# Kernel tuning notes

Measured on AMD Instinct MI355X. Metric: run time of the kernel, lower is better.

The kernel has to match this reference:

```python
import jax, jax.numpy as jnp
import numpy as np
import math

EPS = 1e-8
H, DM, S = 16, 1024, 128  # heads, d_model, seq_len (== channels)
DK = DM // H


def _fq_act_uint8(x):
    # Brevitas Uint8ActPerTensorFloat: per-tensor unsigned 8-bit fake-quant (negatives clip to 0)
    s = jnp.maximum(jnp.max(x), EPS) / 255.0
    return jnp.clip(jnp.round(x / s), 0.0, 255.0) * s


def _fq_w_int8(w):
    # Int8 weight per-tensor, narrow range [-127, 127]
    s = jnp.maximum(jnp.max(jnp.abs(w)), EPS) / 127.0
    return jnp.clip(jnp.round(w / s), -127.0, 127.0) * s, s


def _fq_pc_int8(x, axis):
    # QuantIdentity: signed 8-bit fake-quant, per-channel scale along `axis` (abs-max stats)
    red = tuple(i for i in range(x.ndim) if i != axis)
    s = jnp.maximum(jnp.max(jnp.abs(x), axis=red, keepdims=True), EPS) / 127.0
    return jnp.clip(jnp.round(x / s), -128.0, 127.0) * s


def _quant_linear(x, W, b):
    # QuantLinear: uint8 input quant, int8 weight quant, Int32 bias quant (scale = s_in * s_w)
    s_in = jnp.maximum(jnp.max(x), EPS) / 255.0
    xq = jnp.clip(jnp.round(x / s_in), 0.0, 255.0) * s_in
    Wq, s_w = _fq_w_int8(W)
    s_b = s_in * s_w
    bq = jnp.round(b / s_b) * s_b
    return jnp.einsum('bsd,od->bso', xq, Wq) + bq


def setup_inputs() -> dict:
    key = jax.random.key(0)
    ks = jax.random.split(key, 12)
    B = 64
    std = 1.0 / math.sqrt(DM)
    inp = {
        'query': jax.random.normal(ks[0], (B, S, DM), jnp.float32),
        'key':   jax.random.normal(ks[1], (B, S, DM), jnp.float32),
        'value': jax.random.normal(ks[2], (B, S, DM), jnp.float32),
        'mask':  jnp.ones((B, S, S), jnp.int32),
    }
    for i, nm in enumerate(['q', 'k', 'v', 'o']):
        inp[f'W{nm}'] = jax.random.normal(ks[3 + i], (DM, DM), jnp.float32) * std
        inp[f'b{nm}'] = jax.random.normal(ks[7 + i], (DM,), jnp.float32) * 0.01
    return inp


def reference(query, key, value, mask, Wq, bq, Wk, bk, Wv, bv, Wo, bo):
    B = query.shape[0]
    # QuantLinear projections -> [B, h, S, d_k]
    def proj(x, W, b):
        return _quant_linear(x, W, b).reshape(B, S, H, DK).transpose(0, 2, 1, 3)
    q = proj(query, Wq, bq)
    k = proj(key, Wk, bk)
    v = proj(value, Wv, bv)

    # quantizer_1: per-channel on q rows (axis 2); quantizer_2: on k^T columns (axis 3)
    kt = jnp.swapaxes(k, -2, -1)  # [B, h, d_k, S]
    scores = jnp.matmul(_fq_pc_int8(q, 2), _fq_pc_int8(kt, 3)) / math.sqrt(DK)
    scores = jnp.where(mask[:, None, :, :] == 0, -1e9, scores)
    p_attn = jax.nn.softmax(scores, axis=-1)

    # quantizer_3: per-channel on p_attn columns (axis 3); quantizer_4: on v rows (axis 2)
    x = jnp.matmul(_fq_pc_int8(p_attn, 3), _fq_pc_int8(v, 2))  # [B, h, S, d_k]
    x = x.transpose(0, 2, 1, 3).reshape(B, S, DM)
    return _quant_linear(x, Wo, bo)
```

## Files before the change

### kernel.cpp

```cpp
#include <hip/hip_runtime.h>
#include <hip/hip_bf16.h>
#include <math.h>

typedef unsigned short u16;
typedef unsigned int u32;
typedef unsigned long long u64;
typedef signed char i8;

constexpr int NB = 64, NS = 128, NDM = 1024, NH = 16, NDK = 64;
constexpr int NM = NB * NS;
constexpr float QEPS = 1e-8f;

typedef __attribute__((ext_vector_type(8))) short short8;
typedef __attribute__((ext_vector_type(4))) float f32x4;
typedef __attribute__((ext_vector_type(4))) int i32x4;

__device__ __forceinline__ u32 fenc(float f) {
  u32 u = __float_as_uint(f);
  return (u & 0x80000000u) ? ~u : (u | 0x80000000u);
}
__device__ __forceinline__ float fdec(u32 u) {
  u = (u & 0x80000000u) ? (u & 0x7FFFFFFFu) : ~u;
  return __uint_as_float(u);
}
__device__ __forceinline__ u16 f2bf(float f) { return (u16)(__float_as_uint(f) >> 16); }
__device__ __forceinline__ float bf2f(u16 u) { return __uint_as_float(((u32)u) << 16); }

__device__ __forceinline__ void glds16(const void* g, void* l) {
  __builtin_amdgcn_global_load_lds(
      (const __attribute__((address_space(1))) void*)(unsigned long long)(uintptr_t)g,
      (__attribute__((address_space(3))) void*)(u32)(uintptr_t)l, 16, 0, 0);
}


__global__ void init_kernel(u32* scl) {
  for (int i = threadIdx.x; i < 2048; i += blockDim.x) scl[i] = 0u;
}

__global__ void maskbits_kernel(const int* __restrict__ mask, u64* __restrict__ mb) {
  int row = blockIdx.x * 4 + (threadIdx.x >> 6);
  int lane = threadIdx.x & 63;
  const int* mrow = mask + (size_t)row * NS;
  u64 b0 = __ballot(mrow[lane] != 0);
  u64 b1 = __ballot(mrow[64 + lane] != 0);
  if (lane == 0) { mb[row * 2] = b0; mb[row * 2 + 1] = b1; }
}

__global__ void fused_max_kernel(const float* __restrict__ q, const float* __restrict__ k,
                                 const float* __restrict__ v, const float* __restrict__ w0,
                                 const float* __restrict__ w1, const float* __restrict__ w2,
                                 const float* __restrict__ w3, u32* __restrict__ sclu) {
  int y = blockIdx.y;
  const float* src; size_t n4; int ab;
  switch (y) {
    case 0: src = q; n4 = (size_t)NM * NDM / 4; ab = 0; break;
    case 1: src = k; n4 = (size_t)NM * NDM / 4; ab = 0; break;
    case 2: src = v; n4 = (size_t)NM * NDM / 4; ab = 0; break;
    case 3: src = w0; n4 = (size_t)NDM * NDM / 4; ab = 1; break;
    case 4: src = w1; n4 = (size_t)NDM * NDM / 4; ab = 1; break;
    case 5: src = w2; n4 = (size_t)NDM * NDM / 4; ab = 1; break;
    default: src = w3; n4 = (size_t)NDM * NDM / 4; ab = 1; break;
  }
  float m = -INFINITY;
  size_t stride = (size_t)gridDim.x * blockDim.x;
  for (size_t i = (size_t)blockIdx.x * blockDim.x + threadIdx.x; i < n4; i += stride) {
    float4 f = ((const float4*)src)[i];
    if (ab) { f.x = fabsf(f.x); f.y = fabsf(f.y); f.z = fabsf(f.z); f.w = fabsf(f.w); }
    m = fmaxf(m, fmaxf(fmaxf(f.x, f.y), fmaxf(f.z, f.w)));
  }
  for (int off = 32; off; off >>= 1) m = fmaxf(m, __shfl_down(m, off));
  __shared__ float sm[4];
  if ((threadIdx.x & 63) == 0) sm[threadIdx.x >> 6] = m;
  __syncthreads();
  if (threadIdx.x == 0) {
    float r = fmaxf(fmaxf(sm[0], sm[1]), fmaxf(sm[2], sm[3]));
    atomicMax(&sclu[y], fenc(r));
  }
}

__global__ __launch_bounds__(256)
void quant_w_i8_kernel(const float* __restrict__ w0, const float* __restrict__ w1,
                       const float* __restrict__ w2, const float* __restrict__ w3,
                       i8* __restrict__ dst, int* __restrict__ colsum,
                       const u32* __restrict__ sclu) {
  int y = blockIdx.y, row = blockIdx.x, tid = threadIdx.x;
  const float* src = (y == 0 ? w0 : y == 1 ? w1 : y == 2 ? w2 : w3) + (size_t)row * NDM;
  float s = fmaxf(fdec(sclu[3 + y]), QEPS) / 127.0f;
  float4 f = ((const float4*)src)[tid];
  int a = (int)fminf(fmaxf(rintf(f.x / s), -127.f), 127.f);
  int b = (int)fminf(fmaxf(rintf(f.y / s), -127.f), 127.f);
  int c = (int)fminf(fmaxf(rintf(f.z / s), -127.f), 127.f);
  int d = (int)fminf(fmaxf(rintf(f.w / s), -127.f), 127.f);
  ((int*)(dst + (size_t)y * NDM * NDM + (size_t)row * NDM))[tid] =
      (a & 255) | ((b & 255) << 8) | ((c & 255) << 16) | ((d & 255) << 24);
  int ssum = a + b + c + d;
  for (int off = 32; off; off >>= 1) ssum += __shfl_down(ssum, off);
  __shared__ int sm[4];
  if ((tid & 63) == 0) sm[tid >> 6] = ssum;
  __syncthreads();
  if (tid == 0) colsum[y * NDM + row] = sm[0] + sm[1] + sm[2] + sm[3];
}

__global__ void quant_a_kernel(const float* __restrict__ s0, const float* __restrict__ s1,
                               const float* __restrict__ s2, i8* __restrict__ dst,
                               const u32* __restrict__ sclu, int slot_base) {
  int y = blockIdx.y;
  const float* src = y == 0 ? s0 : y == 1 ? s1 : s2;
  i8* d = dst + (size_t)y * NM * NDM;
  float s = fmaxf(fdec(sclu[slot_base + y]), QEPS) / 255.0f;
  size_t n4 = (size_t)NM * NDM / 4;
  size_t stride = (size_t)gridDim.x * blockDim.x;
  for (size_t i = (size_t)blockIdx.x * blockDim.x + threadIdx.x; i < n4; i += stride) {
    float4 f = ((const float4*)src)[i];
    int a = (int)fminf(fmaxf(rintf(f.x / s), 0.f), 255.f) - 128;
    int b = (int)fminf(fmaxf(rintf(f.y / s), 0.f), 255.f) - 128;
    int c = (int)fminf(fmaxf(rintf(f.z / s), 0.f), 255.f) - 128;
    int e = (int)fminf(fmaxf(rintf(f.w / s), 0.f), 255.f) - 128;
    ((int*)d)[i] = (a & 255) | ((b & 255) << 8) | ((c & 255) << 16) | ((e & 255) << 24);
  }
}

__global__ void qkv_i8_kernel(const float* __restrict__ projbase, i8* __restrict__ dstbase,
                              const float* __restrict__ scl) {
  int y = blockIdx.y;
  const float* src = projbase + (size_t)y * NM * NDM;
  i8* dst = dstbase + (size_t)y * NM * NDM;
  const float* sb = scl + 8 + y * 128;
  size_t n4 = (size_t)NM * NDM / 4;
  size_t stride = (size_t)gridDim.x * blockDim.x;
  for (size_t i = (size_t)blockIdx.x * blockDim.x + threadIdx.x; i < n4; i += stride) {
    int s_idx = (int)((i >> 8) & 127);
    float s = fmaxf(sb[s_idx], QEPS) / 127.0f;
    float4 f = ((const float4*)src)[i];
    int a = (int)fminf(fmaxf(rintf(f.x / s), -128.f), 127.f);
    int b = (int)fminf(fmaxf(rintf(f.y / s), -128.f), 127.f);
    int c = (int)fminf(fmaxf(rintf(f.z / s), -128.f), 127.f);
    int d = (int)fminf(fmaxf(rintf(f.w / s), -128.f), 127.f);
    ((int*)dst)[i] = (a & 255) | ((b & 255) << 8) | ((c & 255) << 16) | ((d & 255) << 24);
  }
}

constexpr int BM = 128, BN = 128, BK = 64;

template <bool PROJ>
__global__ __launch_bounds__(256)
void gemm_kernel(const i8* __restrict__ Abase, const i8* __restrict__ Wbase,
                 const int* __restrict__ colsum, const float* __restrict__ b0,
                 const float* __restrict__ b1, const float* __restrict__ b2,
                 float* __restrict__ Cbase, u32* __restrict__ sclu) {
  constexpr int K = NDM, N = NDM;
  const int z = PROJ ? blockIdx.z : 0;
  const i8* A = Abase + (size_t)z * NM * NDM;
  const i8* Wt = PROJ ? (Wbase + (size_t)z * NDM * NDM) : Wbase;
  const float* bias = PROJ ? (z == 0 ? b0 : z == 1 ? b1 : b2) : b0;
  float* C = PROJ ? (Cbase + (size_t)z * NM * NDM) : Cbase;
  const u32* slot_in = PROJ ? (sclu + z) : (sclu + 7);
  const u32* slot_w = PROJ ? (sclu + 3 + z) : (sclu + 6);
  const int* cs = colsum + (PROJ ? z : 3) * NDM;

  __shared__ __align__(16) i8 As[BM][BK];
  __shared__ __align__(16) i8 Bs[BN][BK];
  __shared__ float rmax2[2][BM];

  const int tid = threadIdx.x;
  const int lane = tid & 63, wave = tid >> 6;
  const int wm = (wave & 1) * 64, wn = (wave >> 1) * 64;
  const int r16 = lane & 15, quad = lane >> 4;
  const int bm = blockIdx.x * BM, bn = blockIdx.y * BN;

  i32x4 acc[4][4] = {};

  const int lrow = lane >> 2, lcol = (lane & 3) * 16;
  for (int k0 = 0; k0 < K; k0 += BK) {
    __syncthreads();
#pragma unroll
    for (int p = 0; p < 2; p++) {
      int r = wave * 32 + p * 16;
      glds16(A + (size_t)(bm + r + lrow) * K + k0 + lcol, &As[r][0]);
      glds16(Wt + (size_t)(bn + r + lrow) * K + k0 + lcol, &Bs[r][0]);
    }
    __syncthreads();
    i32x4 af[4], bfr[4];
#pragma unroll
    for (int i = 0; i < 4; i++) af[i] = *(const i32x4*)(&As[wm + i * 16 + r16][quad * 16]);
#pragma unroll
    for (int j = 0; j < 4; j++) bfr[j] = *(const i32x4*)(&Bs[wn + j * 16 + r16][quad * 16]);
#pragma unroll
    for (int i = 0; i < 4; i++)
#pragma unroll
      for (int j = 0; j < 4; j++)
        acc[i][j] = __builtin_amdgcn_mfma_i32_16x16x64_i8(af[i], bfr[j], acc[i][j], 0, 0, 0);
  }

  float s_in = fmaxf(fdec(*slot_in), QEPS) / 255.0f;
  float s_w = fmaxf(fdec(*slot_w), QEPS) / 127.0f;
  float sc = s_in * s_w;

  float bq[4];
  int csj[4];
#pragma unroll
  for (int j = 0; j < 4; j++) {
    int gc = bn + wn + j * 16 + r16;
    bq[j] = rintf(bias[gc] / sc) * sc;
    csj[j] = cs[gc] << 7;
  }
#pragma unroll
  for (int i = 0; i < 4; i++) {
#pragma unroll
    for (int r = 0; r < 4; r++) {
      int lr = wm + i * 16 + quad * 4 + r;
      int gr = bm + lr;
      float rm = 0.0f;
#pragma unroll
      for (int j = 0; j < 4; j++) {
        int gc = bn + wn + j * 16 + r16;
        float val = (float)(acc[i][j][r] + csj[j]) * sc + bq[j];
        C[(size_t)gr * N + gc] = val;
        if (PROJ) rm = fmaxf(rm, fabsf(val));
      }
      if (PROJ) {
#pragma unroll
        for (int off = 1; off < 16; off <<= 1) rm = fmaxf(rm, __shfl_xor(rm, off));
        if (r16 == 0) rmax2[wave >> 1][lr] = rm;
      }
    }
  }
  if (PROJ) {
    __syncthreads();
    if (tid < BM) {
      float m = fmaxf(rmax2[0][tid], rmax2[1][tid]);
      atomicMax((int*)&sclu[8 + z * 128 + tid], __float_as_int(m));
    }
  }
}

__global__ __launch_bounds__(256)
void attn_scores_kernel(const i8* __restrict__ qi8, const i8* __restrict__ ki8,
                        const u64* __restrict__ mb, const float* __restrict__ scl,
                        u32* __restrict__ sclu, float* __restrict__ Pn) {
  const int bh = blockIdx.x, b = bh >> 4, h = bh & 15;
  const int tid = threadIdx.x, lane = tid & 63, wave = tid >> 6;
  const int r16 = lane & 15, quad = lane >> 4;

  __shared__ __align__(16) i8 Qs[NS][80];
  __shared__ __align__(16) i8 Ks[NS][80];
  __shared__ float sqv[NS], skv[NS];
  __shared__ float cmw[4][NS];

  {
    int row = tid >> 1, half = (tid & 1) * 32;
    const i8* qp = qi8 + (size_t)(b * NS + row) * NDM + h * NDK + half;
    const i8* kp = ki8 + (size_t)(b * NS + row) * NDM + h * NDK + half;
    *(int4*)&Qs[row][half] = *(const int4*)qp;
    *(int4*)&Qs[row][half + 16] = *(const int4*)(qp + 16);
    *(int4*)&Ks[row][half] = *(const int4*)kp;
    *(int4*)&Ks[row][half + 16] = *(const int4*)(kp + 16);
    if (tid < NS) {
      sqv[tid] = fmaxf(scl[8 + tid], QEPS) / 127.0f;
      skv[tid] = fmaxf(scl[8 + 128 + tid], QEPS) / 127.0f;
    }
  }
  __syncthreads();

  const int rowbase = wave * 32;
  i32x4 acc[2][8] = {};
#pragma unroll
  for (int mt = 0; mt < 2; mt++) {
    i32x4 a = *(const i32x4*)&Qs[rowbase + mt * 16 + r16][quad * 16];
#pragma unroll
    for (int nt = 0; nt < 8; nt++) {
      i32x4 bfrag = *(const i32x4*)&Ks[nt * 16 + r16][quad * 16];
      acc[mt][nt] = __builtin_amdgcn_mfma_i32_16x16x64_i8(a, bfrag, acc[mt][nt], 0, 0, 0);
    }
  }

  float skc[8], cm[8];
#pragma unroll
  for (int nt = 0; nt < 8; nt++) { skc[nt] = skv[nt * 16 + r16]; cm[nt] = 0.0f; }

#pragma unroll
  for (int mt = 0; mt < 2; mt++) {
#pragma unroll
    for (int r = 0; r < 4; r++) {
      int row = rowbase + mt * 16 + quad * 4 + r;
      float sq = sqv[row];
      const u64* mrow = mb + ((size_t)b * NS + row) * 2;
      u64 m0 = mrow[0], m1 = mrow[1];
      float vals[8];
      float mx = -INFINITY;
#pragma unroll
      for (int nt = 0; nt < 8; nt++) {
        float v = (float)acc[mt][nt][r] * (sq * skc[nt]) * 0.125f;
        u64 bits = nt < 4 ? m0 : m1;
        if (((bits >> ((nt * 16 + r16) & 63)) & 1ull) == 0) v = -1e9f;
        vals[nt] = v;
        mx = fmaxf(mx, v);
      }
#pragma unroll
      for (int off = 1; off < 16; off <<= 1) mx = fmaxf(mx, __shfl_xor(mx, off));
      float sum = 0.0f;
#pragma unroll
      for (int nt = 0; nt < 8; nt++) { vals[nt] = __expf(vals[nt] - mx); sum += vals[nt]; }
#pragma unroll
      for (int off = 1; off < 16; off <<= 1) sum += __shfl_xor(sum, off);
      float* prow = Pn + ((size_t)bh * NS + row) * NS;
#pragma unroll
      for (int nt = 0; nt < 8; nt++) {
        float p = vals[nt] / sum;
        prow[nt * 16 + r16] = p;
        cm[nt] = fmaxf(cm[nt], p);
      }
    }
  }

#pragma unroll
  for (int nt = 0; nt < 8; nt++) {
    float c = cm[nt];
    c = fmaxf(c, __shfl_xor(c, 16));
    c = fmaxf(c, __shfl_xor(c, 32));
    if (quad == 0) cmw[wave][nt * 16 + r16] = c;
  }
  __syncthreads();
  if (tid < NS) {
    float c = fmaxf(fmaxf(cmw[0][tid], cmw[1][tid]), fmaxf(cmw[2][tid], cmw[3][tid]));
    atomicMax((int*)&sclu[392 + tid], __float_as_int(c));
  }
}

__global__ __launch_bounds__(256)
void attn_pv_kernel(const float* __restrict__ Pn, const i8* __restrict__ vi8,
                    const float* __restrict__ scl, float* __restrict__ xout,
                    u32* __restrict__ xmax_slot) {
  const int bh = blockIdx.x, b = bh >> 4, h = bh & 15;
  const int tid = threadIdx.x, lane = tid & 63, wave = tid >> 6;
  const int r16 = lane & 15, quad = lane >> 4;
  const int rowbase = wave * 32;

  __shared__ __align__(16) u16 Ps[NS][72];
  __shared__ __align__(16) u16 Vhi[64][72];
  __shared__ __align__(16) u16 Vlo[64][72];
  __shared__ float spv[NS], svv[NS];

  if (tid < NS) {
    spv[tid] = fmaxf(scl[392 + tid], QEPS) / 127.0f;
    svv[tid] = fmaxf(scl[8 + 256 + tid], QEPS) / 127.0f;
  }

  f32x4 xacc[2][4] = {};
  for (int half = 0; half < 2; half++) {
    __syncthreads();
    {
      int row = tid >> 1, jl0 = (tid & 1) * 32;
      const float* prow = Pn + ((size_t)bh * NS + row) * NS + half * 64 + jl0;
#pragma unroll
      for (int c4 = 0; c4 < 8; c4++) {
        float4 p = *(const float4*)(prow + c4 * 4);
        int j = half * 64 + jl0 + c4 * 4;
        ushort4 o;
        o.x = f2bf(fminf(fmaxf(rintf(p.x / spv[j + 0]), -128.f), 127.f));
        o.y = f2bf(fminf(fmaxf(rintf(p.y / spv[j + 1]), -128.f), 127.f));
        o.z = f2bf(fminf(fmaxf(rintf(p.z / spv[j + 2]), -128.f), 127.f));
        o.w = f2bf(fminf(fmaxf(rintf(p.w / spv[j + 3]), -128.f), 127.f));
        *(ushort4*)&Ps[row][jl0 + c4 * 4] = o;
      }
    }
    {
      int jl = tid >> 2, d0 = (tid & 3) * 16;
      int j = half * 64 + jl;
      float g = spv[j] * svv[j];
      const i8* vp = vi8 + (size_t)(b * NS + j) * NDM + h * NDK + d0;
      int4 raw = *(const int4*)vp;
      const i8* rb = (const i8*)&raw;
#pragma unroll
      for (int d = 0; d < 16; d++) {
        float w = (float)rb[d] * g;
        u16 hi = f2bf(w);
        Vhi[d0 + d][jl] = hi;
        Vlo[d0 + d][jl] = f2bf(w - bf2f(hi));
      }
    }
    __syncthreads();
#pragma unroll
    for (int kk = 0; kk < 2; kk++) {
      short8 pa[2];
#pragma unroll
      for (int mt = 0; mt < 2; mt++)
        pa[mt] = *(const short8*)&Ps[rowbase + mt * 16 + r16][kk * 32 + quad * 8];
#pragma unroll
      for (int nt = 0; nt < 4; nt++) {
        short8 vh = *(const short8*)&Vhi[nt * 16 + r16][kk * 32 + quad * 8];
        short8 vl = *(const short8*)&Vlo[nt * 16 + r16][kk * 32 + quad * 8];
#pragma unroll
        for (int mt = 0; mt < 2; mt++) {
          xacc[mt][nt] = __builtin_amdgcn_mfma_f32_16x16x32_bf16(pa[mt], vh, xacc[mt][nt], 0, 0, 0);
          xacc[mt][nt] = __builtin_amdgcn_mfma_f32_16x16x32_bf16(pa[mt], vl, xacc[mt][nt], 0, 0, 0);
        }
      }
    }
  }

  float mx = -INFINITY;
#pragma unroll
  for (int mt = 0; mt < 2; mt++)
#pragma unroll
    for (int nt = 0; nt < 4; nt++)
#pragma unroll
      for (int r = 0; r < 4; r++) {
        int row = rowbase + mt * 16 + quad * 4 + r;
        xout[((size_t)b * NS + row) * NDM + h * NDK + nt * 16 + r16] = xacc[mt][nt][r];
        mx = fmaxf(mx, xacc[mt][nt][r]);
      }
#pragma unroll
  for (int off = 1; off < 64; off <<= 1) mx = fmaxf(mx, __shfl_xor(mx, off));
  if (lane == 0) atomicMax(xmax_slot, fenc(mx));
}

constexpr size_t OFF_SCL = 0;
constexpr size_t OFF_CS  = 8192;
constexpr size_t OFF_MB  = OFF_CS + 4 * NDM * 4;
constexpr size_t OFF_W   = OFF_MB + (size_t)NM * 16;
constexpr size_t OFF_XQ  = OFF_W + 4 * (size_t)NDM * NDM;
constexpr size_t OFF_PQ  = OFF_XQ + 3 * (size_t)NM * NDM;
constexpr size_t OFF_I8  = OFF_PQ + 3 * (size_t)NM * NDM * 4;

extern "C" void kernel_launch(void* const* d_in, const int* in_sizes, int n_in,
                              void* d_out, int out_size, void* d_ws, size_t ws_size,
                              hipStream_t stream) {
  const float* query = (const float*)d_in[0];
  const float* key = (const float*)d_in[1];
  const float* value = (const float*)d_in[2];
  const int* mask = (const int*)d_in[3];
  const float* Wq = (const float*)d_in[4]; const float* bq = (const float*)d_in[5];
  const float* Wk = (const float*)d_in[6]; const float* bk = (const float*)d_in[7];
  const float* Wv = (const float*)d_in[8]; const float* bv = (const float*)d_in[9];
  const float* Wo = (const float*)d_in[10]; const float* bo = (const float*)d_in[11];

  char* ws = (char*)d_ws;
  float* scl = (float*)(ws + OFF_SCL);
  u32* sclu = (u32*)scl;
  int* colsum = (int*)(ws + OFF_CS);
  u64* mb = (u64*)(ws + OFF_MB);
  i8* wb = (i8*)(ws + OFF_W);
  i8* wob = wb + 3 * (size_t)NDM * NDM;
  i8* xq = (i8*)(ws + OFF_XQ);
  float* proj = (float*)(ws + OFF_PQ);
  i8* qkv8 = (i8*)(ws + OFF_I8);
  float* Pn = proj;
  float* xout = proj + 2 * (size_t)NM * NDM;
  i8* vi8 = qkv8 + 2 * (size_t)NM * NDM;

  init_kernel<<<1, 256, 0, stream>>>(sclu);
  maskbits_kernel<<<NM / 4, 256, 0, stream>>>(mask, mb);
  fused_max_kernel<<<dim3(512, 7), 256, 0, stream>>>(query, key, value, Wq, Wk, Wv, Wo, sclu);
  quant_w_i8_kernel<<<dim3(NDM, 4), 256, 0, stream>>>(Wq, Wk, Wv, Wo, wb, colsum, sclu);
  quant_a_kernel<<<dim3(512, 3), 256, 0, stream>>>(query, key, value, xq, sclu, 0);

  gemm_kernel<true><<<dim3(NM / BM, NDM / BN, 3), 256, 0, stream>>>(
      xq, wb, colsum, bq, bk, bv, proj, sclu);

  qkv_i8_kernel<<<dim3(512, 3), 256, 0, stream>>>(proj, qkv8, scl);

  attn_scores_kernel<<<NB * NH, 256, 0, stream>>>(qkv8, qkv8 + (size_t)NM * NDM, mb, scl,
                                                  sclu, Pn);
  attn_pv_kernel<<<NB * NH, 256, 0, stream>>>(Pn, vi8, scl, xout, sclu + 7);

  quant_a_kernel<<<dim3(512, 1), 256, 0, stream>>>(xout, xout, xout, xq, sclu, 7);
  gemm_kernel<false><<<dim3(NM / BM, NDM / BN, 1), 256, 0, stream>>>(
      xq, wob, colsum, bo, bo, bo, (float*)d_out, sclu);
}
```

Baseline: 431.3 us.

## Rewrite int8 GEMM as single-wave triple-buffered tiles; fuse qkv quant into attention

The int8 GEMM changes from a 4-wave 128x128 block with two barriers per K step to a single-wave 64x64 block. That block streams A and W through a triple-buffered LDS ring using vmcnt waits instead of barriers, and its block index is swizzled across XCDs. The separate qkv int8 quantize pass is removed, and the attention kernels now quantize q/k/v from the fp32 projections as they load them. The init and mask-bit kernels are merged into one launch and the quant_a grid is widened. This trades a full extra memory pass and launches for redundant fp32 reads and per-row atomics in the GEMM epilogue.

```diff
diff --git a/kernel.cpp b/kernel.cpp
--- a/kernel.cpp
+++ b/kernel.cpp
@@ -32,12 +32,13 @@
       (__attribute__((address_space(3))) void*)(u32)(uintptr_t)l, 16, 0, 0);
 }
 
-
-__global__ void init_kernel(u32* scl) {
-  for (int i = threadIdx.x; i < 2048; i += blockDim.x) scl[i] = 0u;
-}
-
-__global__ void maskbits_kernel(const int* __restrict__ mask, u64* __restrict__ mb) {
+constexpr int WCNT(int vm) { return (vm & 15) | ((vm >> 4) << 14) | (7 << 4) | (15 << 8); }
+
+
+__global__ void initmask_kernel(const int* __restrict__ mask, u64* __restrict__ mb,
+                                u32* __restrict__ scl) {
+  if (blockIdx.x == 0)
+    for (int i = threadIdx.x; i < 2048; i += 256) scl[i] = 0u;
   int row = blockIdx.x * 4 + (threadIdx.x >> 6);
   int lane = threadIdx.x & 63;
   const int* mrow = mask + (size_t)row * NS;
@@ -120,124 +121,107 @@
   }
 }
 
-__global__ void qkv_i8_kernel(const float* __restrict__ projbase, i8* __restrict__ dstbase,
-                              const float* __restrict__ scl) {
-  int y = blockIdx.y;
-  const float* src = projbase + (size_t)y * NM * NDM;
-  i8* dst = dstbase + (size_t)y * NM * NDM;
-  const float* sb = scl + 8 + y * 128;
-  size_t n4 = (size_t)NM * NDM / 4;
-  size_t stride = (size_t)gridDim.x * blockDim.x;
-  for (size_t i = (size_t)blockIdx.x * blockDim.x + threadIdx.x; i < n4; i += stride) {
-    int s_idx = (int)((i >> 8) & 127);
-    float s = fmaxf(sb[s_idx], QEPS) / 127.0f;
-    float4 f = ((const float4*)src)[i];
-    int a = (int)fminf(fmaxf(rintf(f.x / s), -128.f), 127.f);
-    int b = (int)fminf(fmaxf(rintf(f.y / s), -128.f), 127.f);
-    int c = (int)fminf(fmaxf(rintf(f.z / s), -128.f), 127.f);
-    int d = (int)fminf(fmaxf(rintf(f.w / s), -128.f), 127.f);
-    ((int*)dst)[i] = (a & 255) | ((b & 255) << 8) | ((c & 255) << 16) | ((d & 255) << 24);
-  }
-}
-
-constexpr int BM = 128, BN = 128, BK = 64;
+constexpr int GBK = 64, NITER = NDM / GBK;
 
 template <bool PROJ>
-__global__ __launch_bounds__(256)
+__global__ __launch_bounds__(64)
 void gemm_kernel(const i8* __restrict__ Abase, const i8* __restrict__ Wbase,
                  const int* __restrict__ colsum, const float* __restrict__ b0,
                  const float* __restrict__ b1, const float* __restrict__ b2,
                  float* __restrict__ Cbase, u32* __restrict__ sclu) {
-  constexpr int K = NDM, N = NDM;
-  const int z = PROJ ? blockIdx.z : 0;
-  const i8* A = Abase + (size_t)z * NM * NDM;
-  const i8* Wt = PROJ ? (Wbase + (size_t)z * NDM * NDM) : Wbase;
+  int id = blockIdx.x;
+  int xcd = id & 7, s = id >> 3;
+  int z = PROJ ? (s >> 8) : 0;
+  int r = PROJ ? (s & 255) : s;
+  int bm = ((r >> 4) * 8 + xcd) * 64;
+  int wn = (r & 15) * 64;
+
+  const i8* A = Abase + (size_t)z * NM * NDM + (size_t)bm * NDM;
+  const i8* W = Wbase + (PROJ ? (size_t)z * NDM * NDM : 0) + (size_t)wn * NDM;
+  float* C = Cbase + (PROJ ? (size_t)z * NM * NDM : 0);
   const float* bias = PROJ ? (z == 0 ? b0 : z == 1 ? b1 : b2) : b0;
-  float* C = PROJ ? (Cbase + (size_t)z * NM * NDM) : Cbase;
-  const u32* slot_in = PROJ ? (sclu + z) : (sclu + 7);
-  const u32* slot_w = PROJ ? (sclu + 3 + z) : (sclu + 6);
   const int* cs = colsum + (PROJ ? z : 3) * NDM;
 
-  __shared__ __align__(16) i8 As[BM][BK];
-  __shared__ __align__(16) i8 Bs[BN][BK];
-  __shared__ float rmax2[2][BM];
-
-  const int tid = threadIdx.x;
-  const int lane = tid & 63, wave = tid >> 6;
-  const int wm = (wave & 1) * 64, wn = (wave >> 1) * 64;
+  __shared__ __align__(16) i8 Ab[3][64 * GBK];
+  __shared__ __align__(16) i8 Bb[3][64 * GBK];
+
+  const int lane = threadIdx.x;
   const int r16 = lane & 15, quad = lane >> 4;
-  const int bm = blockIdx.x * BM, bn = blockIdx.y * BN;
+  const int lrow = lane >> 2, lcol = (lane & 3) * 16;
+
+  auto stage = [&](int k, int buf) {
+#pragma unroll
+    for (int p = 0; p < 4; p++) {
+      glds16(A + (size_t)(p * 16 + lrow) * NDM + k * GBK + lcol, &Ab[buf][p * 1024]);
+      glds16(W + (size_t)(p * 16 + lrow) * NDM + k * GBK + lcol, &Bb[buf][p * 1024]);
+    }
+  };
+  stage(0, 0);
+  stage(1, 1);
 
   i32x4 acc[4][4] = {};
-
-  const int lrow = lane >> 2, lcol = (lane & 3) * 16;
-  for (int k0 = 0; k0 < K; k0 += BK) {
-    __syncthreads();
-#pragma unroll
-    for (int p = 0; p < 2; p++) {
-      int r = wave * 32 + p * 16;
-      glds16(A + (size_t)(bm + r + lrow) * K + k0 + lcol, &As[r][0]);
-      glds16(Wt + (size_t)(bn + r + lrow) * K + k0 + lcol, &Bs[r][0]);
-    }
-    __syncthreads();
-    i32x4 af[4], bfr[4];
-#pragma unroll
-    for (int i = 0; i < 4; i++) af[i] = *(const i32x4*)(&As[wm + i * 16 + r16][quad * 16]);
-#pragma unroll
-    for (int j = 0; j < 4; j++) bfr[j] = *(const i32x4*)(&Bs[wn + j * 16 + r16][quad * 16]);
+  int bufr = 0, bufc = 2;
+  for (int k = 0; k < NITER; k++) {
+    if (k + 2 < NITER) stage(k + 2, bufc);
+    if (k < NITER - 2)      __builtin_amdgcn_s_waitcnt(WCNT(16));
+    else if (k == NITER - 2) __builtin_amdgcn_s_waitcnt(WCNT(8));
+    else                     __builtin_amdgcn_s_waitcnt(WCNT(0));
+    const i8* ab = &Ab[bufr][0];
+    const i8* bb = &Bb[bufr][0];
+    i32x4 af[4], bf[4];
+#pragma unroll
+    for (int t = 0; t < 4; t++) {
+      af[t] = *(const i32x4*)(ab + (t * 16 + r16) * GBK + quad * 16);
+      bf[t] = *(const i32x4*)(bb + (t * 16 + r16) * GBK + quad * 16);
+    }
 #pragma unroll
     for (int i = 0; i < 4; i++)
 #pragma unroll
       for (int j = 0; j < 4; j++)
-        acc[i][j] = __builtin_amdgcn_mfma_i32_16x16x64_i8(af[i], bfr[j], acc[i][j], 0, 0, 0);
-  }
-
-  float s_in = fmaxf(fdec(*slot_in), QEPS) / 255.0f;
-  float s_w = fmaxf(fdec(*slot_w), QEPS) / 127.0f;
+        acc[i][j] = __builtin_amdgcn_mfma_i32_16x16x64_i8(af[i], bf[j], acc[i][j], 0, 0, 0);
+    bufr = bufr == 2 ? 0 : bufr + 1;
+    bufc = bufc == 2 ? 0 : bufc + 1;
+  }
+
+  float s_in = fmaxf(fdec(sclu[PROJ ? z : 7]), QEPS) / 255.0f;
+  float s_w = fmaxf(fdec(sclu[PROJ ? 3 + z : 6]), QEPS) / 127.0f;
   float sc = s_in * s_w;
 
   float bq[4];
   int csj[4];
 #pragma unroll
   for (int j = 0; j < 4; j++) {
-    int gc = bn + wn + j * 16 + r16;
+    int gc = wn + j * 16 + r16;
     bq[j] = rintf(bias[gc] / sc) * sc;
-    csj[j] = cs[gc] << 7;
+    csj[j] = cs[gc] * 128;
   }
 #pragma unroll
   for (int i = 0; i < 4; i++) {
 #pragma unroll
-    for (int r = 0; r < 4; r++) {
-      int lr = wm + i * 16 + quad * 4 + r;
-      int gr = bm + lr;
+    for (int rr = 0; rr < 4; rr++) {
+      int row = bm + i * 16 + quad * 4 + rr;
       float rm = 0.0f;
 #pragma unroll
       for (int j = 0; j < 4; j++) {
-        int gc = bn + wn + j * 16 + r16;
-        float val = (float)(acc[i][j][r] + csj[j]) * sc + bq[j];
-        C[(size_t)gr * N + gc] = val;
+        int gc = wn + j * 16 + r16;
+        float val = (float)(acc[i][j][rr] + csj[j]) * sc + bq[j];
+        C[(size_t)row * NDM + gc] = val;
         if (PROJ) rm = fmaxf(rm, fabsf(val));
       }
       if (PROJ) {
 #pragma unroll
         for (int off = 1; off < 16; off <<= 1) rm = fmaxf(rm, __shfl_xor(rm, off));
-        if (r16 == 0) rmax2[wave >> 1][lr] = rm;
-      }
-    }
-  }
-  if (PROJ) {
-    __syncthreads();
-    if (tid < BM) {
-      float m = fmaxf(rmax2[0][tid], rmax2[1][tid]);
-      atomicMax((int*)&sclu[8 + z * 128 + tid], __float_as_int(m));
+        if (r16 == 0)
+          atomicMax((int*)&sclu[8 + z * 128 + (row & 127)], __float_as_int(rm));
+      }
     }
   }
 }
 
 __global__ __launch_bounds__(256)
-void attn_scores_kernel(const i8* __restrict__ qi8, const i8* __restrict__ ki8,
-                        const u64* __restrict__ mb, const float* __restrict__ scl,
-                        u32* __restrict__ sclu, float* __restrict__ Pn) {
+void attn_scores_kernel(const float* __restrict__ proj, const u64* __restrict__ mb,
+                        const float* __restrict__ scl, u32* __restrict__ sclu,
+                        float* __restrict__ Pn) {
   const int bh = blockIdx.x, b = bh >> 4, h = bh & 15;
   const int tid = threadIdx.x, lane = tid & 63, wave = tid >> 6;
   const int r16 = lane & 15, quad = lane >> 4;
@@ -248,13 +232,31 @@
   __shared__ float cmw[4][NS];
 
   {
-    int row = tid >> 1, half = (tid & 1) * 32;
-    const i8* qp = qi8 + (size_t)(b * NS + row) * NDM + h * NDK + half;
-    const i8* kp = ki8 + (size_t)(b * NS + row) * NDM + h * NDK + half;
-    *(int4*)&Qs[row][half] = *(const int4*)qp;
-    *(int4*)&Qs[row][half + 16] = *(const int4*)(qp + 16);
-    *(int4*)&Ks[row][half] = *(const int4*)kp;
-    *(int4*)&Ks[row][half + 16] = *(const int4*)(kp + 16);
+    int row = tid >> 1, hf = (tid & 1) * 32;
+    float sq = fmaxf(scl[8 + row], QEPS) / 127.0f;
+    float sk = fmaxf(scl[8 + 128 + row], QEPS) / 127.0f;
+    const float* qp = proj + ((size_t)b * NS + row) * NDM + h * NDK + hf;
+    const float* kp = proj + (size_t)NM * NDM + ((size_t)b * NS + row) * NDM + h * NDK + hf;
+    int qw[8], kw[8];
+#pragma unroll
+    for (int c = 0; c < 8; c++) {
+      float4 qf = *(const float4*)(qp + c * 4);
+      float4 kf = *(const float4*)(kp + c * 4);
+      int q0 = (int)fminf(fmaxf(rintf(qf.x / sq), -128.f), 127.f);
+      int q1 = (int)fminf(fmaxf(rintf(qf.y / sq), -128.f), 127.f);
+      int q2 = (int)fminf(fmaxf(rintf(qf.z / sq), -128.f), 127.f);
+      int q3 = (int)fminf(fmaxf(rintf(qf.w / sq), -128.f), 127.f);
+      qw[c] = (q0 & 255) | ((q1 & 255) << 8) | ((q2 & 255) << 16) | ((q3 & 255) << 24);
+      int k0 = (int)fminf(fmaxf(rintf(kf.x / sk), -128.f), 127.f);
+      int k1 = (int)fminf(fmaxf(rintf(kf.y / sk), -128.f), 127.f);
+      int k2 = (int)fminf(fmaxf(rintf(kf.z / sk), -128.f), 127.f);
+      int k3 = (int)fminf(fmaxf(rintf(kf.w / sk), -128.f), 127.f);
+      kw[c] = (k0 & 255) | ((k1 & 255) << 8) | ((k2 & 255) << 16) | ((k3 & 255) << 24);
+    }
+    *(int4*)&Qs[row][hf] = *(int4*)&qw[0];
+    *(int4*)&Qs[row][hf + 16] = *(int4*)&qw[4];
+    *(int4*)&Ks[row][hf] = *(int4*)&kw[0];
+    *(int4*)&Ks[row][hf + 16] = *(int4*)&kw[4];
     if (tid < NS) {
       sqv[tid] = fmaxf(scl[8 + tid], QEPS) / 127.0f;
       skv[tid] = fmaxf(scl[8 + 128 + tid], QEPS) / 127.0f;
@@ -281,8 +283,8 @@
 #pragma unroll
   for (int mt = 0; mt < 2; mt++) {
 #pragma unroll
-    for (int r = 0; r < 4; r++) {
-      int row = rowbase + mt * 16 + quad * 4 + r;
+    for (int rr = 0; rr < 4; rr++) {
+      int row = rowbase + mt * 16 + quad * 4 + rr;
       float sq = sqv[row];
       const u64* mrow = mb + ((size_t)b * NS + row) * 2;
       u64 m0 = mrow[0], m1 = mrow[1];
@@ -290,7 +292,7 @@
       float mx = -INFINITY;
 #pragma unroll
       for (int nt = 0; nt < 8; nt++) {
-        float v = (float)acc[mt][nt][r] * (sq * skc[nt]) * 0.125f;
+        float v = (float)acc[mt][nt][rr] * (sq * skc[nt]) * 0.125f;
         u64 bits = nt < 4 ? m0 : m1;
         if (((bits >> ((nt * 16 + r16) & 63)) & 1ull) == 0) v = -1e9f;
         vals[nt] = v;
@@ -328,7 +330,7 @@
 }
 
 __global__ __launch_bounds__(256)
-void attn_pv_kernel(const float* __restrict__ Pn, const i8* __restrict__ vi8,
+void attn_pv_kernel(const float* __restrict__ Pn, const float* __restrict__ projv,
                     const float* __restrict__ scl, float* __restrict__ xout,
                     u32* __restrict__ xmax_slot) {
   const int bh = blockIdx.x, b = bh >> 4, h = bh & 15;
@@ -367,16 +369,24 @@
     {
       int jl = tid >> 2, d0 = (tid & 3) * 16;
       int j = half * 64 + jl;
-      float g = spv[j] * svv[j];
-      const i8* vp = vi8 + (size_t)(b * NS + j) * NDM + h * NDK + d0;
-      int4 raw = *(const int4*)vp;
-      const i8* rb = (const i8*)&raw;
-#pragma unroll
-      for (int d = 0; d < 16; d++) {
-        float w = (float)rb[d] * g;
-        u16 hi = f2bf(w);
-        Vhi[d0 + d][jl] = hi;
-        Vlo[d0 + d][jl] = f2bf(w - bf2f(hi));
+      float sv = svv[j];
+      float g = spv[j] * sv;
+      const float* vp = projv + ((size_t)b * NS + j) * NDM + h * NDK + d0;
+#pragma unroll
+      for (int c = 0; c < 4; c++) {
+        float4 vf = *(const float4*)(vp + c * 4);
+        float vq[4];
+        vq[0] = fminf(fmaxf(rintf(vf.x / sv), -128.f), 127.f);
+        vq[1] = fminf(fmaxf(rintf(vf.y / sv), -128.f), 127.f);
+        vq[2] = fminf(fmaxf(rintf(vf.z / sv), -128.f), 127.f);
+        vq[3] = fminf(fmaxf(rintf(vf.w / sv), -128.f), 127.f);
+#pragma unroll
+        for (int t = 0; t < 4; t++) {
+          float w = vq[t] * g;
+          u16 hi = f2bf(w);
+          Vhi[d0 + c * 4 + t][jl] = hi;
+          Vlo[d0 + c * 4 + t][jl] = f2bf(w - bf2f(hi));
+        }
       }
     }
     __syncthreads();
@@ -405,10 +415,10 @@
 #pragma unroll
     for (int nt = 0; nt < 4; nt++)
 #pragma unroll
-      for (int r = 0; r < 4; r++) {
-        int row = rowbase + mt * 16 + quad * 4 + r;
-        xout[((size_t)b * NS + row) * NDM + h * NDK + nt * 16 + r16] = xacc[mt][nt][r];
-        mx = fmaxf(mx, xacc[mt][nt][r]);
+      for (int rr = 0; rr < 4; rr++) {
+        int row = rowbase + mt * 16 + quad * 4 + rr;
+        xout[((size_t)b * NS + row) * NDM + h * NDK + nt * 16 + r16] = xacc[mt][nt][rr];
+        mx = fmaxf(mx, xacc[mt][nt][rr]);
       }
 #pragma unroll
   for (int off = 1; off < 64; off <<= 1) mx = fmaxf(mx, __shfl_xor(mx, off));
@@ -421,7 +431,7 @@
 constexpr size_t OFF_W   = OFF_MB + (size_t)NM * 16;
 constexpr size_t OFF_XQ  = OFF_W + 4 * (size_t)NDM * NDM;
 constexpr size_t OFF_PQ  = OFF_XQ + 3 * (size_t)NM * NDM;
-constexpr size_t OFF_I8  = OFF_PQ + 3 * (size_t)NM * NDM * 4;
+constexpr size_t OFF_PN  = OFF_PQ + 3 * (size_t)NM * NDM * 4;
 
 extern "C" void kernel_launch(void* const* d_in, const int* in_sizes, int n_in,
                               void* d_out, int out_size, void* d_ws, size_t ws_size,
@@ -444,27 +454,21 @@
   i8* wob = wb + 3 * (size_t)NDM * NDM;
   i8* xq = (i8*)(ws + OFF_XQ);
   float* proj = (float*)(ws + OFF_PQ);
-  i8* qkv8 = (i8*)(ws + OFF_I8);
-  float* Pn = proj;
-  float* xout = proj + 2 * (size_t)NM * NDM;
-  i8* vi8 = qkv8 + 2 * (size_t)NM * NDM;
-
-  init_kernel<<<1, 256, 0, stream>>>(sclu);
-  maskbits_kernel<<<NM / 4, 256, 0, stream>>>(mask, mb);
+  float* Pn = (float*)(ws + OFF_PN);
+  float* projv = proj + 2 * (size_t)NM * NDM;
+  float* xout = projv;
+
+  initmask_kernel<<<NM / 4, 256, 0, stream>>>(mask, mb, sclu);
   fused_max_kernel<<<dim3(512, 7), 256, 0, stream>>>(query, key, value, Wq, Wk, Wv, Wo, sclu);
   quant_w_i8_kernel<<<dim3(NDM, 4), 256, 0, stream>>>(Wq, Wk, Wv, Wo, wb, colsum, sclu);
-  quant_a_kernel<<<dim3(512, 3), 256, 0, stream>>>(query, key, value, xq, sclu, 0);
-
-  gemm_kernel<true><<<dim3(NM / BM, NDM / BN, 3), 256, 0, stream>>>(
-      xq, wb, colsum, bq, bk, bv, proj, sclu);
-
-  qkv_i8_kernel<<<dim3(512, 3), 256, 0, stream>>>(proj, qkv8, scl);
-
-  attn_scores_kernel<<<NB * NH, 256, 0, stream>>>(qkv8, qkv8 + (size_t)NM * NDM, mb, scl,
-                                                  sclu, Pn);
-  attn_pv_kernel<<<NB * NH, 256, 0, stream>>>(Pn, vi8, scl, xout, sclu + 7);
-
-  quant_a_kernel<<<dim3(512, 1), 256, 0, stream>>>(xout, xout, xout, xq, sclu, 7);
-  gemm_kernel<false><<<dim3(NM / BM, NDM / BN, 1), 256, 0, stream>>>(
-      xq, wob, colsum, bo, bo, bo, (float*)d_out, sclu);
-}
+  quant_a_kernel<<<dim3(1024, 3), 256, 0, stream>>>(query, key, value, xq, sclu, 0);
+
+  gemm_kernel<true><<<6144, 64, 0, stream>>>(xq, wb, colsum, bq, bk, bv, proj, sclu);
+
+  attn_scores_kernel<<<NB * NH, 256, 0, stream>>>(proj, mb, scl, sclu, Pn);
+  attn_pv_kernel<<<NB * NH, 256, 0, stream>>>(Pn, projv, scl, xout, sclu + 7);
+
+  quant_a_kernel<<<dim3(1024, 1), 256, 0, stream>>>(xout, xout, xout, xq, sclu, 7);
+  gemm_kernel<false><<<2048, 64, 0, stream>>>(xq, wob, colsum, bo, bo, bo,
+                                              (float*)d_out, sclu);
+}
```

Result: slower. 742.1 us (+72.0%).
